# Performance work log

Hardware: AMD Instinct MI355X
Metric: run time of the kernel (lower is better)

Reference implementation:

```python
import jax, jax.numpy as jnp
import numpy as np

N, E = 50000, 800000
F_N, F_E = 32, 16
HC, H, C, L = 128, 2, 64, 3  # hidden_channels, heads, out per head, num_layers
NEG_SLOPE = 0.2  # PyG GATConv default


def setup_inputs() -> dict:
    key = jax.random.key(0)
    ks = jax.random.split(key, 32)
    rn = lambda k, shape, s=0.05: (jax.random.normal(k, shape, jnp.float32) * s)
    return {
        "x": jax.random.normal(ks[0], (N, F_N), jnp.float32),
        "edge_index": jax.random.randint(ks[1], (2, E), 0, N),
        "edge_attr": jax.random.normal(ks[2], (E, F_E), jnp.float32),
        # node encoder: Linear(32,128) -> ReLU -> Linear(128,128)
        "w_n1": rn(ks[3], (F_N, HC)), "b_n1": jnp.zeros((HC,), jnp.float32),
        "w_n2": rn(ks[4], (HC, HC)), "b_n2": jnp.zeros((HC,), jnp.float32),
        # edge encoder: Linear(16,128) -> ReLU (output is ignored by GATConv, edge_dim=None)
        "w_e": rn(ks[5], (F_E, HC)), "b_e": jnp.zeros((HC,), jnp.float32),
        # 3 GATConv layers: lin [128,H*C], att_src/att_dst [H,C], bias [H*C]
        "conv_w": rn(ks[6], (L, HC, H * C)),
        "conv_att_src": rn(ks[7], (L, H, C)),
        "conv_att_dst": rn(ks[8], (L, H, C)),
        "conv_b": jnp.zeros((L, H * C), jnp.float32),
        # path prediction head: Linear(256,128)->ReLU->Linear(128,64)->ReLU->Linear(64,1)->Sigmoid
        "wp1": rn(ks[9], (2 * HC, HC)), "bp1": jnp.zeros((HC,), jnp.float32),
        "wp2": rn(ks[10], (HC, 64)), "bp2": jnp.zeros((64,), jnp.float32),
        "wp3": rn(ks[11], (64, 1)), "bp3": jnp.zeros((1,), jnp.float32),
        # vulnerability head: Linear(128,64)->ReLU->Linear(64,1)->Sigmoid
        "wv1": rn(ks[12], (HC, 64)), "bv1": jnp.zeros((64,), jnp.float32),
        "wv2": rn(ks[13], (64, 1)), "bv2": jnp.zeros((1,), jnp.float32),
    }


def _gat_layer(x, src, dst, w, att_src, att_dst, bias):
    n = x.shape[0]
    h = (x @ w).reshape(n, H, C)                       # [N,H,C]
    a_src = jnp.sum(h * att_src, axis=-1)              # [N,H]
    a_dst = jnp.sum(h * att_dst, axis=-1)              # [N,H]
    alpha = a_src[src] + a_dst[dst]                    # [E',H]
    alpha = jax.nn.leaky_relu(alpha, NEG_SLOPE)
    amax = jax.lax.stop_gradient(jax.ops.segment_max(alpha, dst, num_segments=n))
    ex = jnp.exp(alpha - amax[dst])
    denom = jax.ops.segment_sum(ex, dst, num_segments=n)  # [N,H] (>0: self-loops)
    coef = ex / denom[dst]                             # softmax over incoming edges
    msg = h[src] * coef[:, :, None]                    # [E',H,C]
    out = jax.ops.segment_sum(msg, dst, num_segments=n)
    return out.reshape(n, H * C) + bias


def reference(x, edge_index, edge_attr,
              w_n1, b_n1, w_n2, b_n2, w_e, b_e,
              conv_w, conv_att_src, conv_att_dst, conv_b,
              wp1, bp1, wp2, bp2, wp3, bp3, wv1, bv1, wv2, bv2):
    n = x.shape[0]
    # node encoder (dropout = identity in eval)
    h = jax.nn.relu(x @ w_n1 + b_n1) @ w_n2 + b_n2
    # edge encoder output is computed but ignored by GATConv (edge_dim=None in PyG)
    _edge_emb = jax.nn.relu(edge_attr @ w_e + b_e)
    # add self loops (GATConv default add_self_loops=True)
    loop = jnp.arange(n, dtype=edge_index.dtype)
    src = jnp.concatenate([edge_index[0], loop])
    dst = jnp.concatenate([edge_index[1], loop])
    for l in range(L):
        h = jax.nn.relu(_gat_layer(h, src, dst, conv_w[l], conv_att_src[l], conv_att_dst[l], conv_b[l]))
    g = jnp.mean(h, axis=0, keepdims=True)             # [1,128] graph embedding
    # path head on cat(x[:1], graph_embedding)
    p = jnp.concatenate([h[:1], g], axis=1)            # [1,256]
    p = jax.nn.relu(p @ wp1 + bp1)
    p = jax.nn.relu(p @ wp2 + bp2)
    path = jax.nn.sigmoid(p @ wp3 + bp3)               # [1,1]
    v = jax.nn.relu(h @ wv1 + bv1)
    vuln = jax.nn.sigmoid(v @ wv2 + bv2)               # [N,1]
    esc = jnp.zeros((1, 1), jnp.float32)               # [1,1]
    return (path, vuln, esc)
```

## Files before the change

### kernel.cpp

```cpp
#include <hip/hip_runtime.h>
#include <math.h>

#define HC 128
#define NSLOPE 0.2f

using bf16x8 = __attribute__((ext_vector_type(8))) short;
using f32x4  = __attribute__((ext_vector_type(4))) float;

__device__ __forceinline__ float lrelu(float v){ return v > 0.f ? v : NSLOPE * v; }

__device__ __forceinline__ unsigned short f2bf(float f){
    unsigned int b = __float_as_uint(f);
    b += 0x7FFFu + ((b >> 16) & 1u);
    return (unsigned short)(b >> 16);
}
__device__ __forceinline__ float bf_lo(unsigned int v){ return __uint_as_float(v << 16); }
__device__ __forceinline__ float bf_hi(unsigned int v){ return __uint_as_float(v & 0xFFFF0000u); }
__device__ __forceinline__ float bf1(unsigned short v){ return __uint_as_float((unsigned int)v << 16); }

__global__ void count_kernel(const int* __restrict__ ei, int* __restrict__ cnt,
                             int* __restrict__ rank, int E){
    int e = blockIdx.x * blockDim.x + threadIdx.x;
    if (e < E) rank[e] = atomicAdd(&cnt[ei[E + e]], 1);
}

__global__ __launch_bounds__(256) void scan_part_kernel(
        const int* __restrict__ deg, int* __restrict__ bsum, int n)
{
    int t = threadIdx.x, lane = t & 63, wid = t >> 6;
    int base = blockIdx.x * 1024 + t * 4;
    int s = 0;
    #pragma unroll
    for (int j = 0; j < 4; ++j){ int i = base + j; if (i < n) s += deg[i]; }
    #pragma unroll
    for (int o = 1; o < 64; o <<= 1) s += __shfl_xor(s, o);
    __shared__ int red[4];
    if (lane == 0) red[wid] = s;
    __syncthreads();
    if (t == 0) bsum[blockIdx.x] = red[0] + red[1] + red[2] + red[3];
}

__global__ __launch_bounds__(64) void scan_top_kernel(
        const int* __restrict__ bsum, int* __restrict__ boff, int* __restrict__ rowptr,
        int nb, int n)
{
    int t = threadIdx.x;
    int v = (t < nb) ? bsum[t] : 0;
    int incl = v;
    #pragma unroll
    for (int o = 1; o < 64; o <<= 1){ int u = __shfl_up(incl, o); if (t >= o) incl += u; }
    if (t < nb) boff[t] = incl - v;
    if (t == 63) rowptr[n] = incl;
}

__global__ __launch_bounds__(256) void scan_fin_kernel(
        const int* __restrict__ deg, const int* __restrict__ boff,
        int* __restrict__ rowptr, int n)
{
    int t = threadIdx.x, lane = t & 63, wid = t >> 6;
    int base = blockIdx.x * 1024 + t * 4;
    int d[4]; int s = 0;
    #pragma unroll
    for (int j = 0; j < 4; ++j){ int i = base + j; d[j] = (i < n) ? deg[i] : 0; s += d[j]; }
    int incl = s;
    #pragma unroll
    for (int o = 1; o < 64; o <<= 1){ int u = __shfl_up(incl, o); if (lane >= o) incl += u; }
    __shared__ int wsum[4];
    if (lane == 63) wsum[wid] = incl;
    __syncthreads();
    int off = boff[blockIdx.x] + (incl - s);
    for (int w = 0; w < wid; ++w) off += wsum[w];
    #pragma unroll
    for (int j = 0; j < 4; ++j){
        int i = base + j;
        if (i < n) rowptr[i] = off;
        off += d[j];
    }
}

__global__ __launch_bounds__(256) void scatter_kernel(
        const int* __restrict__ ei, const int* __restrict__ rowptr,
        const int* __restrict__ rank, int* __restrict__ colsrc, int E)
{
    int b = blockIdx.x * 2048 + threadIdx.x;
    int e[8]; bool v[8]; int d[8], s[8], r[8];
    #pragma unroll
    for (int i = 0; i < 8; ++i){ e[i] = b + i * 256; v[i] = e[i] < E; }
    #pragma unroll
    for (int i = 0; i < 8; ++i) if (v[i]){ d[i] = ei[E + e[i]]; s[i] = ei[e[i]]; r[i] = rank[e[i]]; }
    #pragma unroll
    for (int i = 0; i < 8; ++i) if (v[i]) colsrc[rowptr[d[i]] + r[i]] = s[i];
}

__global__ __launch_bounds__(256) void wtrans_all_kernel(
        const float* __restrict__ w_n2, const float* __restrict__ conv_w,
        const float* __restrict__ wv1,
        unsigned short* __restrict__ Wt0, unsigned short* __restrict__ Wt1,
        unsigned short* __restrict__ Wtv)
{
    int idx = blockIdx.x * 256 + threadIdx.x;
    if (idx >= 9216) return;
    const float* Wm; unsigned short* Wo; int C; int rem;
    if (idx < 2048){ Wm = w_n2; Wo = Wt0; C = 128; rem = idx; }
    else if (idx < 8192){
        int m2 = (idx - 2048) >> 11; rem = (idx - 2048) & 2047;
        Wm = conv_w + (size_t)m2 * 16384; Wo = Wt1 + (size_t)m2 * 16384; C = 128;
    } else { rem = idx - 8192; Wm = wv1; Wo = Wtv; C = 64; }
    int c = rem >> 4, kg = rem & 15;
    unsigned int pk[4];
    #pragma unroll
    for (int j = 0; j < 4; ++j){
        float a = Wm[(size_t)(kg*8 + j*2    ) * C + c];
        float b = Wm[(size_t)(kg*8 + j*2 + 1) * C + c];
        pk[j] = (unsigned int)f2bf(a) | ((unsigned int)f2bf(b) << 16);
    }
    *(uint4*)(Wo + (size_t)c * 128 + kg * 8) = make_uint4(pk[0], pk[1], pk[2], pk[3]);
}

__global__ __launch_bounds__(256) void enc1_kernel(
        const float* __restrict__ x, const float* __restrict__ w1, const float* __restrict__ b1,
        unsigned short* __restrict__ hid, int n)
{
    __shared__ float As[32][68];
    __shared__ float Bs[32][128];
    int t = threadIdx.x;
    int m0 = blockIdx.x * 64;
    int tm = t >> 4, tn = t & 15;

    #pragma unroll
    for (int i = 0; i < 2; ++i){
        int f = i * 256 + t;
        int row = f >> 3, kq = f & 7;
        int gr = m0 + row; if (gr > n - 1) gr = n - 1;
        float4 v = *(const float4*)(x + (size_t)gr * 32 + kq * 4);
        As[kq*4+0][row] = v.x; As[kq*4+1][row] = v.y; As[kq*4+2][row] = v.z; As[kq*4+3][row] = v.w;
    }
    #pragma unroll
    for (int i = 0; i < 4; ++i){
        int f = i * 256 + t;
        int kk = f >> 5, nq = f & 31;
        *(float4*)&Bs[kk][nq*4] = *(const float4*)(w1 + (size_t)kk * 128 + nq * 4);
    }
    __syncthreads();

    float acc[4][8];
    #pragma unroll
    for (int i = 0; i < 4; ++i)
        #pragma unroll
        for (int j = 0; j < 8; ++j) acc[i][j] = 0.f;

    #pragma unroll 4
    for (int k = 0; k < 32; ++k){
        float a[4], b[8];
        *(float4*)&a[0] = *(float4*)&As[k][tm*4];
        *(float4*)&b[0] = *(float4*)&Bs[k][tn*8];
        *(float4*)&b[4] = *(float4*)&Bs[k][tn*8+4];
        #pragma unroll
        for (int i = 0; i < 4; ++i)
            #pragma unroll
            for (int j = 0; j < 8; ++j) acc[i][j] = fmaf(a[i], b[j], acc[i][j]);
    }

    float bb[8];
    *(float4*)&bb[0] = *(const float4*)(b1 + tn*8);
    *(float4*)&bb[4] = *(const float4*)(b1 + tn*8 + 4);
    #pragma unroll
    for (int i = 0; i < 4; ++i){
        int node = m0 + tm*4 + i;
        if (node < n){
            float o[8];
            #pragma unroll
            for (int j = 0; j < 8; ++j) o[j] = fmaxf(acc[i][j] + bb[j], 0.f);
            uint4 pk;
            pk.x = (unsigned int)f2bf(o[0]) | ((unsigned int)f2bf(o[1]) << 16);
            pk.y = (unsigned int)f2bf(o[2]) | ((unsigned int)f2bf(o[3]) << 16);
            pk.z = (unsigned int)f2bf(o[4]) | ((unsigned int)f2bf(o[5]) << 16);
            pk.w = (unsigned int)f2bf(o[6]) | ((unsigned int)f2bf(o[7]) << 16);
            *(uint4*)(hid + (size_t)node*HC + tn*8) = pk;
        }
    }
}

template<bool ATT>
__global__ __launch_bounds__(256) void gemm_mfma_kernel(
        const unsigned short* __restrict__ A, const unsigned short* __restrict__ Wt,
        const float* __restrict__ bias,
        const float* __restrict__ att_s, const float* __restrict__ att_d,
        unsigned short* __restrict__ Cb, unsigned char* __restrict__ C8,
        float* __restrict__ asrc, float* __restrict__ adst, int n)
{
    __shared__ float lds[4][16][132];
    int t = threadIdx.x;
    int w = t >> 6, l = t & 63;
    int lane15 = l & 15, lanehi = l >> 4;
    int m0 = blockIdx.x * 64 + w * 16;

    f32x4 acc[8];
    #pragma unroll
    for (int ct = 0; ct < 8; ++ct) acc[ct] = (f32x4){0.f, 0.f, 0.f, 0.f};

    int ar = m0 + lane15; if (ar > n - 1) ar = n - 1;
    const unsigned short* Arow = A + (size_t)ar * HC;

    #pragma unroll
    for (int kc = 0; kc < 4; ++kc){
        bf16x8 af = *reinterpret_cast<const bf16x8*>(Arow + kc * 32 + lanehi * 8);
        #pragma unroll
        for (int ct = 0; ct < 8; ++ct){
            bf16x8 bf = *reinterpret_cast<const bf16x8*>(
                Wt + (size_t)(ct * 16 + lane15) * HC + kc * 32 + lanehi * 8);
            acc[ct] = __builtin_amdgcn_mfma_f32_16x16x32_bf16(af, bf, acc[ct], 0, 0, 0);
        }
    }

    if (ATT){
        float ats[8], atd[8];
        #pragma unroll
        for (int ct = 0; ct < 8; ++ct){
            ats[ct] = att_s[ct * 16 + lane15];
            atd[ct] = att_d[ct * 16 + lane15];
        }
        #pragma unroll
        for (int r = 0; r < 4; ++r){
            float sa0 = 0.f, sd0 = 0.f, sa1 = 0.f, sd1 = 0.f;
            #pragma unroll
            for (int ct = 0; ct < 4; ++ct){
                sa0 = fmaf(acc[ct][r], ats[ct], sa0);
                sd0 = fmaf(acc[ct][r], atd[ct], sd0);
            }
            #pragma unroll
            for (int ct = 4; ct < 8; ++ct){
                sa1 = fmaf(acc[ct][r], ats[ct], sa1);
                sd1 = fmaf(acc[ct][r], atd[ct], sd1);
            }
            #pragma unroll
            for (int o = 1; o < 16; o <<= 1){
                sa0 += __shfl_xor(sa0, o); sd0 += __shfl_xor(sd0, o);
                sa1 += __shfl_xor(sa1, o); sd1 += __shfl_xor(sd1, o);
            }
            int node = m0 + lanehi * 4 + r;
            if (lane15 == 0 && node < n){
                asrc[(size_t)node * 2]     = sa0;
                adst[(size_t)node * 2]     = sd0;
                asrc[(size_t)node * 2 + 1] = sa1;
                adst[(size_t)node * 2 + 1] = sd1;
            }
        }
    }

    float bb[8];
    #pragma unroll
    for (int ct = 0; ct < 8; ++ct) bb[ct] = ATT ? 0.f : bias[ct * 16 + lane15];
    #pragma unroll
    for (int ct = 0; ct < 8; ++ct)
        #pragma unroll
        for (int r = 0; r < 4; ++r)
            lds[w][lanehi * 4 + r][ct * 16 + lane15] = acc[ct][r] + bb[ct];
    __syncthreads();

    int row = lane15, cb = lanehi;
    int node = m0 + row;
    if (node < n){
        if (!ATT){
            #pragma unroll
            for (int q = 0; q < 4; ++q){
                float o[8];
                *(float4*)&o[0] = *(float4*)&lds[w][row][cb * 32 + q * 8];
                *(float4*)&o[4] = *(float4*)&lds[w][row][cb * 32 + q * 8 + 4];
                uint4 pk;
                pk.x = (unsigned int)f2bf(o[0]) | ((unsigned int)f2bf(o[1]) << 16);
                pk.y = (unsigned int)f2bf(o[2]) | ((unsigned int)f2bf(o[3]) << 16);
                pk.z = (unsigned int)f2bf(o[4]) | ((unsigned int)f2bf(o[5]) << 16);
                pk.w = (unsigned int)f2bf(o[6]) | ((unsigned int)f2bf(o[7]) << 16);
                *(uint4*)(Cb + (size_t)node * HC + cb * 32 + q * 8) = pk;
            }
        } else {
            unsigned int words[8];
            #pragma unroll
            for (int gq = 0; gq < 8; ++gq){
                float4 v = *(float4*)&lds[w][row][cb * 32 + gq * 4];
                unsigned int r = __builtin_amdgcn_cvt_pk_fp8_f32(v.x, v.y, 0, 0);
                r = __builtin_amdgcn_cvt_pk_fp8_f32(v.z, v.w, r, 1);
                words[gq] = r;
            }
            *(uint4*)(C8 + (size_t)node * HC + cb * 32)      = make_uint4(words[0], words[1], words[2], words[3]);
            *(uint4*)(C8 + (size_t)node * HC + cb * 32 + 16) = make_uint4(words[4], words[5], words[6], words[7]);
        }
    }
}

__global__ __launch_bounds__(256) void aggregate_kernel(
        const unsigned char* __restrict__ h8, const float* __restrict__ asrc,
        const float* __restrict__ adst,
        const int* __restrict__ rowptr, const int* __restrict__ colsrc,
        const float* __restrict__ bias, unsigned short* __restrict__ hout, int n)
{
    int i = blockIdx.x * 4 + (threadIdx.x >> 6);
    if (i >= n) return;
    int t = threadIdx.x & 63;
    int head = t >> 5;
    float2 adv = *(const float2*)(adst + (size_t)i * 2);
    float2 asv = *(const float2*)(asrc + (size_t)i * 2);
    float ads = head ? adv.y : adv.x;
    float exs = __expf(lrelu((head ? asv.y : asv.x) + ads));
    unsigned int hv = *(const unsigned short*)(h8 + (size_t)i * HC + t * 2);
    float acc0 = exs * __builtin_amdgcn_cvt_f32_fp8(hv, 0);
    float acc1 = exs * __builtin_amdgcn_cvt_f32_fp8(hv, 1);
    float D = exs;

    int e  = rowptr[i];
    int e1 = rowptr[i + 1];
    while (e < e1){
        int m = e1 - e; if (m > 64) m = 64;
        int sl = 0; float ex0 = 0.f, ex1 = 0.f;
        if (t < m){
            sl = colsrc[e + t];
            float2 as = *(const float2*)(asrc + (size_t)sl * 2);
            ex0 = __expf(lrelu(as.x + adv.x));
            ex1 = __expf(lrelu(as.y + adv.y));
        }
        int j = 0;
        for (; j + 8 <= m; j += 8){
            int s[8]; float c[8];
            #pragma unroll
            for (int u = 0; u < 8; ++u){
                s[u] = __shfl(sl, j + u);
                float c0 = __shfl(ex0, j + u);
                float c1 = __shfl(ex1, j + u);
                c[u] = head ? c1 : c0;
            }
            unsigned int v[8];
            #pragma unroll
            for (int u = 0; u < 8; ++u)
                v[u] = *(const unsigned short*)(h8 + (size_t)s[u] * HC + t * 2);
            #pragma unroll
            for (int u = 0; u < 8; ++u){
                acc0 = fmaf(c[u], __builtin_amdgcn_cvt_f32_fp8(v[u], 0), acc0);
                acc1 = fmaf(c[u], __builtin_amdgcn_cvt_f32_fp8(v[u], 1), acc1);
                D += c[u];
            }
        }
        for (; j < m; ++j){
            int s = __shfl(sl, j);
            float c0 = __shfl(ex0, j), c1 = __shfl(ex1, j);
            float c = head ? c1 : c0;
            unsigned int v = *(const unsigned short*)(h8 + (size_t)s * HC + t * 2);
            acc0 = fmaf(c, __builtin_amdgcn_cvt_f32_fp8(v, 0), acc0);
            acc1 = fmaf(c, __builtin_amdgcn_cvt_f32_fp8(v, 1), acc1);
            D += c;
        }
        e += m;
    }
    float rD = 1.0f / D;
    float o0 = fmaxf(acc0 * rD + bias[2*t],     0.f);
    float o1 = fmaxf(acc1 * rD + bias[2*t + 1], 0.f);
    ((unsigned int*)hout)[(size_t)i * 64 + t] =
        (unsigned int)f2bf(o0) | ((unsigned int)f2bf(o1) << 16);
}

__global__ __launch_bounds__(256) void mean_part_kernel(
        const unsigned short* __restrict__ h, float* __restrict__ partial, int n)
{
    int t = threadIdx.x;
    int cq = t & 31;
    int rl = t >> 5;
    float4 acc = make_float4(0.f, 0.f, 0.f, 0.f);
    for (int i = blockIdx.x * 8 + rl; i < n; i += gridDim.x * 8){
        uint2 v = *(const uint2*)(h + (size_t)i * HC + cq * 4);
        acc.x += bf_lo(v.x); acc.y += bf_hi(v.x);
        acc.z += bf_lo(v.y); acc.w += bf_hi(v.y);
    }
    __shared__ float4 red[256];
    red[t] = acc;
    __syncthreads();
    if (t < 128){
        float4 o = red[t + 128];
        red[t].x += o.x; red[t].y += o.y; red[t].z += o.z; red[t].w += o.w;
    }
    __syncthreads();
    if (t < 64){
        float4 o = red[t + 64];
        red[t].x += o.x; red[t].y += o.y; red[t].z += o.z; red[t].w += o.w;
    }
    __syncthreads();
    if (t < 32){
        float4 a = red[t], b = red[t + 32];
        float4 s = make_float4(a.x + b.x, a.y + b.y, a.z + b.z, a.w + b.w);
        *(float4*)(partial + (size_t)blockIdx.x * HC + t * 4) = s;
    }
}

__global__ __launch_bounds__(256) void mean_fin_kernel(
        const float* __restrict__ partial, float* __restrict__ g, int nb)
{
    int t = threadIdx.x;
    int cq = t & 31, b0 = t >> 5;
    float4 acc = make_float4(0.f, 0.f, 0.f, 0.f);
    for (int b = b0; b < nb; b += 8){
        float4 v = *(const float4*)(partial + (size_t)b * HC + cq * 4);
        acc.x += v.x; acc.y += v.y; acc.z += v.z; acc.w += v.w;
    }
    __shared__ float4 red[256];
    red[t] = acc;
    __syncthreads();
    if (t < 128){
        float4 o = red[t + 128];
        red[t].x += o.x; red[t].y += o.y; red[t].z += o.z; red[t].w += o.w;
    }
    __syncthreads();
    if (t < 64){
        float4 o = red[t + 64];
        red[t].x += o.x; red[t].y += o.y; red[t].z += o.z; red[t].w += o.w;
    }
    __syncthreads();
    if (t < 32){
        float4 a = red[t], b = red[t + 32];
        float4 s = make_float4(a.x + b.x, a.y + b.y, a.z + b.z, a.w + b.w);
        *(float4*)(g + t * 4) = s;
    }
}

__global__ __launch_bounds__(256) void vuln_mfma_kernel(
        const unsigned short* __restrict__ h, const unsigned short* __restrict__ Wtv,
        const float* __restrict__ bv1, const float* __restrict__ wv2,
        const float* __restrict__ bv2, float* __restrict__ out, int n)
{
    int t = threadIdx.x;
    int w = t >> 6, l = t & 63;
    int lane15 = l & 15, lanehi = l >> 4;
    int m0 = blockIdx.x * 64 + w * 16;

    f32x4 acc[4];
    #pragma unroll
    for (int ct = 0; ct < 4; ++ct) acc[ct] = (f32x4){0.f, 0.f, 0.f, 0.f};

    int ar = m0 + lane15; if (ar > n - 1) ar = n - 1;
    const unsigned short* Arow = h + (size_t)ar * HC;

    #pragma unroll
    for (int kc = 0; kc < 4; ++kc){
        bf16x8 af = *reinterpret_cast<const bf16x8*>(Arow + kc * 32 + lanehi * 8);
        #pragma unroll
        for (int ct = 0; ct < 4; ++ct){
            bf16x8 bf = *reinterpret_cast<const bf16x8*>(
                Wtv + (size_t)(ct * 16 + lane15) * HC + kc * 32 + lanehi * 8);
            acc[ct] = __builtin_amdgcn_mfma_f32_16x16x32_bf16(af, bf, acc[ct], 0, 0, 0);
        }
    }

    float bb[4], wv[4];
    #pragma unroll
    for (int ct = 0; ct < 4; ++ct){
        bb[ct] = bv1[ct * 16 + lane15];
        wv[ct] = wv2[ct * 16 + lane15];
    }
    float bv2v = bv2[0];
    #pragma unroll
    for (int r = 0; r < 4; ++r){
        float s = 0.f;
        #pragma unroll
        for (int ct = 0; ct < 4; ++ct)
            s = fmaf(fmaxf(acc[ct][r] + bb[ct], 0.f), wv[ct], s);
        #pragma unroll
        for (int o = 1; o < 16; o <<= 1) s += __shfl_xor(s, o);
        int node = m0 + lanehi * 4 + r;
        if (lane15 == 0 && node < n)
            out[1 + node] = 1.0f / (1.0f + __expf(-(s + bv2v)));
    }
}

__global__ __launch_bounds__(128) void path_kernel(
        const unsigned short* __restrict__ h, const float* __restrict__ g,
        const float* __restrict__ wp1, const float* __restrict__ bp1,
        const float* __restrict__ wp2, const float* __restrict__ bp2,
        const float* __restrict__ wp3, const float* __restrict__ bp3,
        float* __restrict__ out, int n)
{
    __shared__ float pc[256];
    __shared__ float p1[HC];
    __shared__ float p2[64];
    int t = threadIdx.x;
    pc[t]       = bf1(h[t]);
    pc[128 + t] = g[t] * (1.0f / (float)n);
    __syncthreads();
    float a = bp1[t];
    for (int k = 0; k < 256; ++k) a = fmaf(pc[k], wp1[k * HC + t], a);
    p1[t] = fmaxf(a, 0.f);
    __syncthreads();
    if (t < 64){
        float a2 = bp2[t];
        for (int k = 0; k < HC; ++k) a2 = fmaf(p1[k], wp2[k * 64 + t], a2);
        p2[t] = fmaxf(a2, 0.f);
    }
    __syncthreads();
    if (t == 0){
        float a3 = bp3[0];
        for (int k = 0; k < 64; ++k) a3 = fmaf(p2[k], wp3[k], a3);
        out[0] = 1.0f / (1.0f + __expf(-a3));
        out[1 + n] = 0.f;
    }
}

extern "C" void kernel_launch(void* const* d_in, const int* in_sizes, int n_in,
                              void* d_out, int out_size, void* d_ws, size_t ws_size,
                              hipStream_t stream)
{
    const float* x    = (const float*)d_in[0];
    const int*   ei   = (const int*)d_in[1];
    const float* w_n1 = (const float*)d_in[3];
    const float* b_n1 = (const float*)d_in[4];
    const float* w_n2 = (const float*)d_in[5];
    const float* b_n2 = (const float*)d_in[6];
    const float* conv_w = (const float*)d_in[9];
    const float* att_s  = (const float*)d_in[10];
    const float* att_d  = (const float*)d_in[11];
    const float* conv_b = (const float*)d_in[12];
    const float* wp1 = (const float*)d_in[13];
    const float* bp1 = (const float*)d_in[14];
    const float* wp2 = (const float*)d_in[15];
    const float* bp2 = (const float*)d_in[16];
    const float* wp3 = (const float*)d_in[17];
    const float* bp3 = (const float*)d_in[18];
    const float* wv1 = (const float*)d_in[19];
    const float* bv1 = (const float*)d_in[20];
    const float* wv2 = (const float*)d_in[21];
    const float* bv2 = (const float*)d_in[22];

    const int N = in_sizes[0] / 32;
    const int E = in_sizes[1] / 2;
    float* out = (float*)d_out;

    char* ws = (char*)d_ws;
    size_t off = 0;
    auto take = [&](size_t bytes) -> char* {
        char* p = ws + off;
        off += (bytes + 255) & ~(size_t)255;
        return p;
    };
    unsigned short* hA = (unsigned short*)take((size_t)N * HC * 2);
    unsigned short* hB = (unsigned short*)take((size_t)N * HC * 2);
    unsigned char*  h8 = (unsigned char*)take((size_t)N * HC);
    float* asrc  = (float*)take((size_t)N * 2 * 4);
    float* adst  = (float*)take((size_t)N * 2 * 4);
    int*   rowptr= (int*)take((size_t)(N + 1) * 4);
    int*   cnt   = (int*)take((size_t)N * 4);
    int*   rank  = (int*)take((size_t)E * 4);
    int*   colsrc= (int*)take((size_t)E * 4);
    float* g     = (float*)take(HC * 4);
    unsigned short* Wt0 = (unsigned short*)take(16384 * 2);
    unsigned short* Wt1 = (unsigned short*)take((size_t)3 * 16384 * 2);
    unsigned short* Wtv = (unsigned short*)take(8192 * 2);
    const int MB = 64;
    float* mpart = (float*)take((size_t)MB * HC * 4);
    int nb = (N + 1023) / 1024;
    int*   bsum  = (int*)take((size_t)((nb + 63) & ~63) * 4);
    int*   boff  = (int*)take((size_t)((nb + 63) & ~63) * 4);

    hipMemsetAsync(cnt, 0, (size_t)N * 4, stream);
    count_kernel<<<(E + 255) / 256, 256, 0, stream>>>(ei, cnt, rank, E);
    scan_part_kernel<<<nb, 256, 0, stream>>>(cnt, bsum, N);
    scan_top_kernel<<<1, 64, 0, stream>>>(bsum, boff, rowptr, nb, N);
    scan_fin_kernel<<<nb, 256, 0, stream>>>(cnt, boff, rowptr, N);
    scatter_kernel<<<(E + 2047) / 2048, 256, 0, stream>>>(ei, rowptr, rank, colsrc, E);

    wtrans_all_kernel<<<36, 256, 0, stream>>>(w_n2, conv_w, wv1, Wt0, Wt1, Wtv);

    int nblk64 = (N + 63) / 64;
    enc1_kernel<<<nblk64, 256, 0, stream>>>(x, w_n1, b_n1, hB, N);
    gemm_mfma_kernel<false><<<nblk64, 256, 0, stream>>>(
        hB, Wt0, b_n2, nullptr, nullptr, hA, nullptr, nullptr, nullptr, N);

    for (int l = 0; l < 3; ++l){
        gemm_mfma_kernel<true><<<nblk64, 256, 0, stream>>>(
            hA, Wt1 + (size_t)l * 16384, nullptr,
            att_s + (size_t)l * HC, att_d + (size_t)l * HC,
            nullptr, h8, asrc, adst, N);
        aggregate_kernel<<<(N + 3) / 4, 256, 0, stream>>>(
            h8, asrc, adst, rowptr, colsrc, conv_b + (size_t)l * HC, hA, N);
    }

    mean_part_kernel<<<MB, 256, 0, stream>>>(hA, mpart, N);
    mean_fin_kernel<<<1, 256, 0, stream>>>(mpart, g, MB);
    vuln_mfma_kernel<<<nblk64, 256, 0, stream>>>(hA, Wtv, bv1, wv2, bv2, out, N);
    path_kernel<<<1, 128, 0, stream>>>(hA, g, wp1, bp1, wp2, bp2, wp3, bp3, out, N);
}
```

Before: 325.4 us.

## Split aggregation wave into four edge groups with 8-byte fp8 gathers

The aggregate kernel now splits each 64-lane wave into four 16-lane groups. Each group handles a different neighbour edge and loads 8 fp8 features per lane with one 8-byte load, where before all 64 lanes handled one edge with 2-byte loads. Partial accumulators are combined with cross-group xor shuffles at the end, and one group writes a packed 16-byte bf16 output. This widens the memory transactions and processes four edges in parallel per wave. In exchange it uses more registers and adds a reduction step, and the tail handling has to mask partial groups.

```diff
diff --git a/kernel.cpp b/kernel.cpp
--- a/kernel.cpp
+++ b/kernel.cpp
@@ -298,15 +298,23 @@
     int i = blockIdx.x * 4 + (threadIdx.x >> 6);
     if (i >= n) return;
     int t = threadIdx.x & 63;
-    int head = t >> 5;
+    int qw = t >> 4;
+    int lc = t & 15;
+    int head = lc >> 3;
     float2 adv = *(const float2*)(adst + (size_t)i * 2);
     float2 asv = *(const float2*)(asrc + (size_t)i * 2);
-    float ads = head ? adv.y : adv.x;
-    float exs = __expf(lrelu((head ? asv.y : asv.x) + ads));
-    unsigned int hv = *(const unsigned short*)(h8 + (size_t)i * HC + t * 2);
-    float acc0 = exs * __builtin_amdgcn_cvt_f32_fp8(hv, 0);
-    float acc1 = exs * __builtin_amdgcn_cvt_f32_fp8(hv, 1);
-    float D = exs;
+    float exs = __expf(lrelu((head ? asv.y : asv.x) + (head ? adv.y : adv.x)));
+    float w0 = (qw == 0) ? exs : 0.f;
+    uint2 hv = *(const uint2*)(h8 + (size_t)i * HC + lc * 8);
+    float a0 = w0 * __builtin_amdgcn_cvt_f32_fp8(hv.x, 0);
+    float a1 = w0 * __builtin_amdgcn_cvt_f32_fp8(hv.x, 1);
+    float a2 = w0 * __builtin_amdgcn_cvt_f32_fp8(hv.x, 2);
+    float a3 = w0 * __builtin_amdgcn_cvt_f32_fp8(hv.x, 3);
+    float a4 = w0 * __builtin_amdgcn_cvt_f32_fp8(hv.y, 0);
+    float a5 = w0 * __builtin_amdgcn_cvt_f32_fp8(hv.y, 1);
+    float a6 = w0 * __builtin_amdgcn_cvt_f32_fp8(hv.y, 2);
+    float a7 = w0 * __builtin_amdgcn_cvt_f32_fp8(hv.y, 3);
+    float D = w0;
 
     int e  = rowptr[i];
     int e1 = rowptr[i + 1];
@@ -321,41 +329,99 @@
         }
         int j = 0;
         for (; j + 8 <= m; j += 8){
-            int s[8]; float c[8];
-            #pragma unroll
-            for (int u = 0; u < 8; ++u){
-                s[u] = __shfl(sl, j + u);
-                float c0 = __shfl(ex0, j + u);
-                float c1 = __shfl(ex1, j + u);
+            int s[2]; float c[2];
+            #pragma unroll
+            for (int u = 0; u < 2; ++u){
+                int src = j + 4 * u + qw;
+                s[u] = __shfl(sl, src);
+                float c0 = __shfl(ex0, src);
+                float c1 = __shfl(ex1, src);
                 c[u] = head ? c1 : c0;
             }
-            unsigned int v[8];
-            #pragma unroll
-            for (int u = 0; u < 8; ++u)
-                v[u] = *(const unsigned short*)(h8 + (size_t)s[u] * HC + t * 2);
-            #pragma unroll
-            for (int u = 0; u < 8; ++u){
-                acc0 = fmaf(c[u], __builtin_amdgcn_cvt_f32_fp8(v[u], 0), acc0);
-                acc1 = fmaf(c[u], __builtin_amdgcn_cvt_f32_fp8(v[u], 1), acc1);
+            uint2 v[2];
+            #pragma unroll
+            for (int u = 0; u < 2; ++u)
+                v[u] = *(const uint2*)(h8 + (size_t)s[u] * HC + lc * 8);
+            #pragma unroll
+            for (int u = 0; u < 2; ++u){
+                a0 = fmaf(c[u], __builtin_amdgcn_cvt_f32_fp8(v[u].x, 0), a0);
+                a1 = fmaf(c[u], __builtin_amdgcn_cvt_f32_fp8(v[u].x, 1), a1);
+                a2 = fmaf(c[u], __builtin_amdgcn_cvt_f32_fp8(v[u].x, 2), a2);
+                a3 = fmaf(c[u], __builtin_amdgcn_cvt_f32_fp8(v[u].x, 3), a3);
+                a4 = fmaf(c[u], __builtin_amdgcn_cvt_f32_fp8(v[u].y, 0), a4);
+                a5 = fmaf(c[u], __builtin_amdgcn_cvt_f32_fp8(v[u].y, 1), a5);
+                a6 = fmaf(c[u], __builtin_amdgcn_cvt_f32_fp8(v[u].y, 2), a6);
+                a7 = fmaf(c[u], __builtin_amdgcn_cvt_f32_fp8(v[u].y, 3), a7);
                 D += c[u];
             }
         }
-        for (; j < m; ++j){
-            int s = __shfl(sl, j);
-            float c0 = __shfl(ex0, j), c1 = __shfl(ex1, j);
+        for (; j + 4 <= m; j += 4){
+            int src = j + qw;
+            int   s  = __shfl(sl, src);
+            float c0 = __shfl(ex0, src);
+            float c1 = __shfl(ex1, src);
             float c = head ? c1 : c0;
-            unsigned int v = *(const unsigned short*)(h8 + (size_t)s * HC + t * 2);
-            acc0 = fmaf(c, __builtin_amdgcn_cvt_f32_fp8(v, 0), acc0);
-            acc1 = fmaf(c, __builtin_amdgcn_cvt_f32_fp8(v, 1), acc1);
+            uint2 v = *(const uint2*)(h8 + (size_t)s * HC + lc * 8);
+            a0 = fmaf(c, __builtin_amdgcn_cvt_f32_fp8(v.x, 0), a0);
+            a1 = fmaf(c, __builtin_amdgcn_cvt_f32_fp8(v.x, 1), a1);
+            a2 = fmaf(c, __builtin_amdgcn_cvt_f32_fp8(v.x, 2), a2);
+            a3 = fmaf(c, __builtin_amdgcn_cvt_f32_fp8(v.x, 3), a3);
+            a4 = fmaf(c, __builtin_amdgcn_cvt_f32_fp8(v.y, 0), a4);
+            a5 = fmaf(c, __builtin_amdgcn_cvt_f32_fp8(v.y, 1), a5);
+            a6 = fmaf(c, __builtin_amdgcn_cvt_f32_fp8(v.y, 2), a6);
+            a7 = fmaf(c, __builtin_amdgcn_cvt_f32_fp8(v.y, 3), a7);
             D += c;
         }
+        if (j < m){
+            int rem = m - j;
+            int src = j + qw;
+            int   s  = __shfl(sl, src);
+            float c0 = __shfl(ex0, src);
+            float c1 = __shfl(ex1, src);
+            float c = head ? c1 : c0;
+            if (qw < rem){
+                uint2 v = *(const uint2*)(h8 + (size_t)s * HC + lc * 8);
+                a0 = fmaf(c, __builtin_amdgcn_cvt_f32_fp8(v.x, 0), a0);
+                a1 = fmaf(c, __builtin_amdgcn_cvt_f32_fp8(v.x, 1), a1);
+                a2 = fmaf(c, __builtin_amdgcn_cvt_f32_fp8(v.x, 2), a2);
+                a3 = fmaf(c, __builtin_amdgcn_cvt_f32_fp8(v.x, 3), a3);
+                a4 = fmaf(c, __builtin_amdgcn_cvt_f32_fp8(v.y, 0), a4);
+                a5 = fmaf(c, __builtin_amdgcn_cvt_f32_fp8(v.y, 1), a5);
+                a6 = fmaf(c, __builtin_amdgcn_cvt_f32_fp8(v.y, 2), a6);
+                a7 = fmaf(c, __builtin_amdgcn_cvt_f32_fp8(v.y, 3), a7);
+                D += c;
+            }
+        }
         e += m;
     }
-    float rD = 1.0f / D;
-    float o0 = fmaxf(acc0 * rD + bias[2*t],     0.f);
-    float o1 = fmaxf(acc1 * rD + bias[2*t + 1], 0.f);
-    ((unsigned int*)hout)[(size_t)i * 64 + t] =
-        (unsigned int)f2bf(o0) | ((unsigned int)f2bf(o1) << 16);
+    a0 += __shfl_xor(a0, 16); a0 += __shfl_xor(a0, 32);
+    a1 += __shfl_xor(a1, 16); a1 += __shfl_xor(a1, 32);
+    a2 += __shfl_xor(a2, 16); a2 += __shfl_xor(a2, 32);
+    a3 += __shfl_xor(a3, 16); a3 += __shfl_xor(a3, 32);
+    a4 += __shfl_xor(a4, 16); a4 += __shfl_xor(a4, 32);
+    a5 += __shfl_xor(a5, 16); a5 += __shfl_xor(a5, 32);
+    a6 += __shfl_xor(a6, 16); a6 += __shfl_xor(a6, 32);
+    a7 += __shfl_xor(a7, 16); a7 += __shfl_xor(a7, 32);
+    D  += __shfl_xor(D, 16);  D  += __shfl_xor(D, 32);
+    if (qw == 0){
+        float rD = 1.0f / D;
+        float4 b0 = *(const float4*)(bias + lc * 8);
+        float4 b1v = *(const float4*)(bias + lc * 8 + 4);
+        float o0 = fmaxf(a0 * rD + b0.x, 0.f);
+        float o1 = fmaxf(a1 * rD + b0.y, 0.f);
+        float o2 = fmaxf(a2 * rD + b0.z, 0.f);
+        float o3 = fmaxf(a3 * rD + b0.w, 0.f);
+        float o4 = fmaxf(a4 * rD + b1v.x, 0.f);
+        float o5 = fmaxf(a5 * rD + b1v.y, 0.f);
+        float o6 = fmaxf(a6 * rD + b1v.z, 0.f);
+        float o7 = fmaxf(a7 * rD + b1v.w, 0.f);
+        uint4 pk;
+        pk.x = (unsigned int)f2bf(o0) | ((unsigned int)f2bf(o1) << 16);
+        pk.y = (unsigned int)f2bf(o2) | ((unsigned int)f2bf(o3) << 16);
+        pk.z = (unsigned int)f2bf(o4) | ((unsigned int)f2bf(o5) << 16);
+        pk.w = (unsigned int)f2bf(o6) | ((unsigned int)f2bf(o7) << 16);
+        *(uint4*)(hout + (size_t)i * HC + lc * 8) = pk;
+    }
 }
 
 __global__ __launch_bounds__(256) void mean_part_kernel(
```

Measured after the change: 309.1 us. 1.05x faster.
